# Kernel optimization log

Measured on AMD Instinct MI355X. Metric: run time of the kernel, lower is better.

Reference implementation:

```python
import jax, jax.numpy as jnp
import numpy as np

T, B, D_IN, H = 512, 256, 512, 128

def setup_inputs() -> dict:
    key = jax.random.key(0)
    ks = jax.random.split(key, 6)
    c0 = jax.random.normal(ks[0], (B, H), jnp.float32)
    h0 = jax.random.normal(ks[1], (B, H), jnp.float32)
    obs = jax.random.normal(ks[2], (T, B, D_IN), jnp.float32)
    done = jax.random.randint(ks[3], (T, B), 0, 2).astype(jnp.bool_)
    Wi = jax.random.normal(ks[4], (D_IN, 4 * H), jnp.float32) * (1.0 / np.sqrt(D_IN))
    Wh = jax.random.normal(ks[5], (H, 4 * H), jnp.float32) * (1.0 / np.sqrt(H))
    b = jnp.zeros((4 * H,), jnp.float32)
    return {"c0": c0, "h0": h0, "obs": obs, "done": done, "Wi": Wi, "Wh": Wh, "b": b}

def reference(c0, h0, obs, done, Wi, Wh, b):
    # Time-scanned flax LSTMCell with done-masked state reset.
    # Carry reset: where(done, initialize_carry()=zeros, old_state).
    # Flax LSTMCell gates (order i,f,g,o): sigmoid/sigmoid/tanh/sigmoid,
    # dense_i has no bias, dense_h has bias b.
    def step(carry, inp):
        c, h = carry
        x, d = inp                      # x: [B, D_IN], d: [B]
        keep = jnp.logical_not(d)[:, None]
        c = jnp.where(keep, c, 0.0)
        h = jnp.where(keep, h, 0.0)
        gates = x @ Wi + h @ Wh + b     # [B, 4H]
        i, f, g, o = jnp.split(gates, 4, axis=-1)
        new_c = jax.nn.sigmoid(f) * c + jax.nn.sigmoid(i) * jnp.tanh(g)
        new_h = jax.nn.sigmoid(o) * jnp.tanh(new_c)
        return (new_c, new_h), new_h

    (cT, hT), ys = jax.lax.scan(step, (c0, h0), (obs, done))
    return ys, cT, hT
```

## Files before the change

### kernel.cpp

```cpp
#include <hip/hip_runtime.h>
#include <hip/hip_bf16.h>
#include <cstdint>
#include <cstddef>

#define TT  512
#define BB  256
#define DIN 512
#define HH  128
#define NG  512

typedef __bf16 bf16x8 __attribute__((ext_vector_type(8)));
typedef float  f32x4  __attribute__((ext_vector_type(4)));

__device__ __forceinline__ float p_recip1p(float e) {
  float s = __builtin_fmaf(2.f, e, -1.f);
  float p = __builtin_fmaf(s, -0.00336424f, 0.00980413f);
  p = __builtin_fmaf(s, p, -0.0243654f);
  p = __builtin_fmaf(s, p, 0.0734565f);
  p = __builtin_fmaf(s, p, -0.222261f);
  p = __builtin_fmaf(s, p, 0.666706f);
  return p;
}
__device__ __forceinline__ float fast_sig(float x) {
  float e = __builtin_amdgcn_exp2f(-1.44269504f * __builtin_fabsf(x));
  float p = p_recip1p(e);
  return x >= 0.f ? p : 1.f - p;
}
__device__ __forceinline__ float fast_tanh(float x) {
  float e = __builtin_amdgcn_exp2f(-2.88539008f * __builtin_fabsf(x));
  float t = __builtin_fmaf(2.f, p_recip1p(e), -1.f);
  return __builtin_copysignf(t, x);
}

__device__ __forceinline__ void lgkm_barrier() {
  asm volatile("s_waitcnt lgkmcnt(0)\n\ts_barrier" ::: "memory");
}

__global__ void wconv_kernel(const float* __restrict__ Wi, const float* __restrict__ Wh,
                             __bf16* __restrict__ WiT, __bf16* __restrict__ WhT) {
  int idx = blockIdx.x * 256 + threadIdx.x;
  if (idx < DIN * NG) {
    int n = idx >> 9, k = idx & 511;
    WiT[(size_t)n * DIN + k] = (__bf16)Wi[(size_t)k * NG + n];
  }
  if (idx < HH * NG) {
    int n = idx >> 7, k = idx & 127;
    WhT[(size_t)n * HH + k] = (__bf16)Wh[(size_t)k * NG + n];
  }
}

__global__ __launch_bounds__(512, 2)
void gemm_kernel(const float* __restrict__ obs, const __bf16* __restrict__ WiT,
                 const float* __restrict__ bias, __bf16* __restrict__ Xg) {
  __shared__ __bf16 Alds[128][40];
  const int tid  = threadIdx.x;
  const int wave = tid >> 6, lane = tid & 63;
  const int l15  = lane & 15, q = lane >> 4;
  const size_t m0 = (size_t)blockIdx.x * 128;

  const f32x4 fzero = {0.f, 0.f, 0.f, 0.f};
  f32x4 acc[8][4];
#pragma unroll
  for (int i = 0; i < 8; i++)
#pragma unroll
    for (int jj = 0; jj < 4; jj++) acc[i][jj] = fzero;

  const int am = tid >> 2, aq = tid & 3;
  const float* aptr = obs + (m0 + am) * DIN + aq * 8;
  const __bf16* bptr[4];
#pragma unroll
  for (int nt = 0; nt < 4; nt++)
    bptr[nt] = WiT + (size_t)(wave * 64 + nt * 16 + l15) * DIN + q * 8;

  float4 a0[2], a1[2];
  bf16x8 bs[2][4];
  a0[0] = *(const float4*)(aptr);      a1[0] = *(const float4*)(aptr + 4);
  a0[1] = *(const float4*)(aptr + 32); a1[1] = *(const float4*)(aptr + 36);
#pragma unroll
  for (int nt = 0; nt < 4; nt++) {
    bs[0][nt] = *(const bf16x8*)(bptr[nt]);
    bs[1][nt] = *(const bf16x8*)(bptr[nt] + 32);
  }

#pragma unroll
  for (int kc = 0; kc < DIN; kc += 32) {
    const int sl = (kc >> 5) & 1;
    if (kc) lgkm_barrier();
    {
      float4 f0 = a0[sl], f1 = a1[sl];
      bf16x8 v = {(__bf16)f0.x, (__bf16)f0.y, (__bf16)f0.z, (__bf16)f0.w,
                  (__bf16)f1.x, (__bf16)f1.y, (__bf16)f1.z, (__bf16)f1.w};
      *(bf16x8*)&Alds[am][aq * 8] = v;
    }
    lgkm_barrier();
    int kp = kc + 64; if (kp > DIN - 32) kp = DIN - 32;
    a0[sl] = *(const float4*)(aptr + kp);
    a1[sl] = *(const float4*)(aptr + kp + 4);
#pragma unroll
    for (int mt = 0; mt < 8; mt++) {
      bf16x8 af = *(const bf16x8*)&Alds[mt * 16 + l15][q * 8];
#pragma unroll
      for (int nt = 0; nt < 4; nt++)
        acc[mt][nt] = __builtin_amdgcn_mfma_f32_16x16x32_bf16(af, bs[sl][nt], acc[mt][nt], 0, 0, 0);
    }
#pragma unroll
    for (int nt = 0; nt < 4; nt++)
      bs[sl][nt] = *(const bf16x8*)(bptr[nt] + kp);
  }

  const int t = blockIdx.x >> 1;
  const int half = blockIdx.x & 1;
#pragma unroll
  for (int mt = 0; mt < 8; mt++) {
    const int bg = half * 8 + mt;
#pragma unroll
    for (int nt = 0; nt < 4; nt++) {
      const int n = wave * 64 + nt * 16 + l15;
      const int g = n >> 7, jj = n & 127;
      const float bb = bias[n];
      __bf16* base = Xg + (size_t)(t * 16 + bg) * 4 * 2048 + jj * 16 + q * 4 + g;
#pragma unroll
      for (int r = 0; r < 4; r++)
        base[(size_t)r * 2048] = (__bf16)(acc[mt][nt][r] + bb);
    }
  }
}

template<int R0>
__device__ __forceinline__ void scan_body(
    const __bf16* __restrict__ Xg, const __bf16* __restrict__ WhT,
    const int* __restrict__ done, const float* __restrict__ c0,
    const float* __restrict__ h0, float* __restrict__ out,
    int bg, __bf16 (*hlds)[16][HH + 8]) {
  const int tid  = threadIdx.x;
  const int wave = tid >> 6, lane = tid & 63;
  const int l15  = lane & 15, q = lane >> 4;
  const int b0 = bg * 16;
  const int j  = wave * 16 + l15;
  const int b  = b0 + q * 4 + R0;
  const int row = q * 4 + R0;

  bf16x8 bfrag[4][4];
#pragma unroll
  for (int g = 0; g < 4; g++)
#pragma unroll
    for (int ks = 0; ks < 4; ks++)
      bfrag[g][ks] = *(const bf16x8*)(WhT + (size_t)(g * HH + j) * HH + ks * 32 + q * 8);

  for (int i = tid; i < 2 * 16 * (HH + 8); i += 512) ((__bf16*)hlds)[i] = (__bf16)0.f;
  __syncthreads();
  const int d0 = done[b];
  float c = c0[(size_t)b * HH + j];
  hlds[0][row][j] = d0 ? (__bf16)0.f : (__bf16)h0[(size_t)b * HH + j];
  __syncthreads();

  const size_t tstride = (size_t)16 * 4 * 2048;
  const __bf16* xpA = Xg + (size_t)(bg * 4 + R0) * 2048 + j * 16 + q * 4;
  const __bf16* xpB = xpA + tstride;
  const int* dpA = done + b;
  const int* dpB = dpA + BB;
  uint2 xgA = *(const uint2*)xpA;  xpA += 2 * tstride;
  uint2 xgB = *(const uint2*)xpB;  xpB += 2 * tstride;
  int dnA = *dpA; dpA += 2 * BB;
  int dnB = *dpB; dpB += 2 * BB;

  const f32x4 fz = {0.f, 0.f, 0.f, 0.f};
  float* op = out + (size_t)b * HH + j;
  float nh = 0.f;

  for (int t = 0; t < TT; t += 2) {
    {
      uint2 xg_c = xgA; int dn_c = dnA, dn_w = dnB;
      if (t + 2 < TT) { xgA = *(const uint2*)xpA; dnA = *dpA; }
      xpA += 2 * tstride; dpA += 2 * BB;

      bf16x8 af[4];
#pragma unroll
      for (int ks = 0; ks < 4; ks++)
        af[ks] = *(const bf16x8*)&hlds[0][l15][ks * 32 + q * 8];
      union { uint2 u; __bf16 h[4]; } ux; ux.u = xg_c;
      f32x4 acc[4];
#pragma unroll
      for (int g = 0; g < 4; g++) {
        float xv = (float)ux.h[g];
        acc[g] = (f32x4){xv, xv, xv, xv};
#pragma unroll
        for (int ks = 0; ks < 4; ks++)
          acc[g] = __builtin_amdgcn_mfma_f32_16x16x32_bf16(af[ks], bfrag[g][ks], acc[g], 0, 0, 0);
      }
      float gi = acc[0][R0], gf = acc[1][R0], gg = acc[2][R0], go = acc[3][R0];
      float cprev = dn_c ? 0.f : c;
      float nc = __builtin_fmaf(fast_sig(gf), cprev, fast_sig(gi) * fast_tanh(gg));
      nh = fast_sig(go) * fast_tanh(nc);
      c = nc;
      *op = nh; op += BB * HH;
      hlds[1][row][j] = dn_w ? (__bf16)0.f : (__bf16)nh;
      lgkm_barrier();
    }
    {
      uint2 xg_c = xgB; int dn_c = dnB, dn_w = dnA;
      if (t + 3 < TT) { xgB = *(const uint2*)xpB; dnB = *dpB; }
      xpB += 2 * tstride; dpB += 2 * BB;

      bf16x8 af[4];
#pragma unroll
      for (int ks = 0; ks < 4; ks++)
        af[ks] = *(const bf16x8*)&hlds[1][l15][ks * 32 + q * 8];
      union { uint2 u; __bf16 h[4]; } ux; ux.u = xg_c;
      f32x4 acc[4];
#pragma unroll
      for (int g = 0; g < 4; g++) {
        float xv = (float)ux.h[g];
        acc[g] = (f32x4){xv, xv, xv, xv};
#pragma unroll
        for (int ks = 0; ks < 4; ks++)
          acc[g] = __builtin_amdgcn_mfma_f32_16x16x32_bf16(af[ks], bfrag[g][ks], acc[g], 0, 0, 0);
      }
      float gi = acc[0][R0], gf = acc[1][R0], gg = acc[2][R0], go = acc[3][R0];
      float cprev = dn_c ? 0.f : c;
      float nc = __builtin_fmaf(fast_sig(gf), cprev, fast_sig(gi) * fast_tanh(gg));
      nh = fast_sig(go) * fast_tanh(nc);
      c = nc;
      *op = nh; op += BB * HH;
      hlds[0][row][j] = dn_w ? (__bf16)0.f : (__bf16)nh;
      lgkm_barrier();
    }
  }
  (void)fz;

  float* cT = out + (size_t)TT * BB * HH;
  float* hT = cT + (size_t)BB * HH;
  cT[(size_t)b * HH + j] = c;
  hT[(size_t)b * HH + j] = nh;
}

__global__ __launch_bounds__(512, 2)
void scan_kernel(const __bf16* __restrict__ Xg, const __bf16* __restrict__ WhT,
                 const int* __restrict__ done, const float* __restrict__ c0,
                 const float* __restrict__ h0, float* __restrict__ out) {
  __shared__ __bf16 hlds[2][16][HH + 8];
  const int bg = blockIdx.x >> 2;
  switch (blockIdx.x & 3) {
    case 0: scan_body<0>(Xg, WhT, done, c0, h0, out, bg, hlds); break;
    case 1: scan_body<1>(Xg, WhT, done, c0, h0, out, bg, hlds); break;
    case 2: scan_body<2>(Xg, WhT, done, c0, h0, out, bg, hlds); break;
    case 3: scan_body<3>(Xg, WhT, done, c0, h0, out, bg, hlds); break;
  }
}

extern "C" void kernel_launch(void* const* d_in, const int* in_sizes, int n_in,
                              void* d_out, int out_size, void* d_ws, size_t ws_size,
                              hipStream_t stream) {
  const float* c0   = (const float*)d_in[0];
  const float* h0   = (const float*)d_in[1];
  const float* obs  = (const float*)d_in[2];
  const int*   done = (const int*)d_in[3];
  const float* Wi   = (const float*)d_in[4];
  const float* Wh   = (const float*)d_in[5];
  const float* bias = (const float*)d_in[6];
  float* out = (float*)d_out;

  char* ws = (char*)d_ws;
  __bf16* Xg  = (__bf16*)ws;
  __bf16* WiT = (__bf16*)(ws + (size_t)134217728);
  __bf16* WhT = (__bf16*)(ws + (size_t)134217728 + 524288);

  wconv_kernel<<<dim3(1024), dim3(256), 0, stream>>>(Wi, Wh, WiT, WhT);
  gemm_kernel<<<dim3(1024), dim3(512), 0, stream>>>(obs, WiT, bias, Xg);
  scan_kernel<<<dim3(64), dim3(512), 0, stream>>>(Xg, WhT, done, c0, h0, out);
}
```

Before: 799.5 us.

## Fuse input GEMM and recurrent scan into one kernel with per-timestep flags

Merges the input-projection GEMM and the recurrent scan into one launch. The first 64 blocks run the scan and spin on per-timestep atomic counters that the GEMM blocks increment after writing their slice of Xg. This lets the serial scan start while the GEMM is still producing later timesteps, hiding most of the GEMM behind the scan. It also swaps the polynomial sigmoid/tanh for exp plus hardware reciprocal and splits the MFMA accumulation into two independent chains to shorten the dependency. The cost is a reliance on scan blocks being resident alongside GEMM blocks (deadlock risk if they are not) and extra atomic-load overhead on each step.

Result: faster. 774.1 us (-3.2%).

```diff
diff --git a/kernel.cpp b/kernel.cpp
--- a/kernel.cpp
+++ b/kernel.cpp
@@ -12,33 +12,37 @@
 typedef __bf16 bf16x8 __attribute__((ext_vector_type(8)));
 typedef float  f32x4  __attribute__((ext_vector_type(4)));
 
-__device__ __forceinline__ float p_recip1p(float e) {
-  float s = __builtin_fmaf(2.f, e, -1.f);
-  float p = __builtin_fmaf(s, -0.00336424f, 0.00980413f);
-  p = __builtin_fmaf(s, p, -0.0243654f);
-  p = __builtin_fmaf(s, p, 0.0734565f);
-  p = __builtin_fmaf(s, p, -0.222261f);
-  p = __builtin_fmaf(s, p, 0.666706f);
-  return p;
-}
 __device__ __forceinline__ float fast_sig(float x) {
-  float e = __builtin_amdgcn_exp2f(-1.44269504f * __builtin_fabsf(x));
-  float p = p_recip1p(e);
-  return x >= 0.f ? p : 1.f - p;
+  float e = __builtin_amdgcn_exp2f(-1.44269504f * x);
+  return __builtin_amdgcn_rcpf(1.f + e);
 }
 __device__ __forceinline__ float fast_tanh(float x) {
-  float e = __builtin_amdgcn_exp2f(-2.88539008f * __builtin_fabsf(x));
-  float t = __builtin_fmaf(2.f, p_recip1p(e), -1.f);
-  return __builtin_copysignf(t, x);
+  float e = __builtin_amdgcn_exp2f(-2.88539008f * x);
+  return __builtin_fmaf(2.f, __builtin_amdgcn_rcpf(1.f + e), -1.f);
 }
 
 __device__ __forceinline__ void lgkm_barrier() {
   asm volatile("s_waitcnt lgkmcnt(0)\n\ts_barrier" ::: "memory");
 }
 
+__device__ __forceinline__ int ld_flag(const int* p) {
+  return __hip_atomic_load(p, __ATOMIC_RELAXED, __HIP_MEMORY_SCOPE_AGENT);
+}
+__device__ __forceinline__ uint2 ld_xg8(const __bf16* p) {
+  unsigned long long v = __hip_atomic_load((const unsigned long long*)p,
+                                           __ATOMIC_RELAXED, __HIP_MEMORY_SCOPE_AGENT);
+  union { unsigned long long u; uint2 v2; } cv; cv.u = v;
+  return cv.v2;
+}
+
 __global__ void wconv_kernel(const float* __restrict__ Wi, const float* __restrict__ Wh,
-                             __bf16* __restrict__ WiT, __bf16* __restrict__ WhT) {
+                             __bf16* __restrict__ WiT, __bf16* __restrict__ WhT,
+                             int* __restrict__ flags) {
   int idx = blockIdx.x * 256 + threadIdx.x;
+  if (blockIdx.x == 0) {
+    flags[threadIdx.x] = 0;
+    flags[threadIdx.x + 256] = 0;
+  }
   if (idx < DIN * NG) {
     int n = idx >> 9, k = idx & 511;
     WiT[(size_t)n * DIN + k] = (__bf16)Wi[(size_t)k * NG + n];
@@ -49,14 +53,14 @@
   }
 }
 
-__global__ __launch_bounds__(512, 2)
-void gemm_kernel(const float* __restrict__ obs, const __bf16* __restrict__ WiT,
-                 const float* __restrict__ bias, __bf16* __restrict__ Xg) {
-  __shared__ __bf16 Alds[128][40];
+__device__ __forceinline__ void gemm_body(
+    const float* __restrict__ obs, const __bf16* __restrict__ WiT,
+    const float* __restrict__ bias, __bf16* __restrict__ Xg,
+    int* __restrict__ flags, int bid, __bf16 (*Alds)[40]) {
   const int tid  = threadIdx.x;
   const int wave = tid >> 6, lane = tid & 63;
   const int l15  = lane & 15, q = lane >> 4;
-  const size_t m0 = (size_t)blockIdx.x * 128;
+  const size_t m0 = (size_t)bid * 128;
 
   const f32x4 fzero = {0.f, 0.f, 0.f, 0.f};
   f32x4 acc[8][4];
@@ -108,8 +112,8 @@
       bs[sl][nt] = *(const bf16x8*)(bptr[nt] + kp);
   }
 
-  const int t = blockIdx.x >> 1;
-  const int half = blockIdx.x & 1;
+  const int t = bid >> 1;
+  const int half = bid & 1;
 #pragma unroll
   for (int mt = 0; mt < 8; mt++) {
     const int bg = half * 8 + mt;
@@ -124,6 +128,12 @@
         base[(size_t)r * 2048] = (__bf16)(acc[mt][nt][r] + bb);
     }
   }
+
+  __syncthreads();
+  if (tid == 0) {
+    __threadfence();
+    __hip_atomic_fetch_add(flags + t, 1, __ATOMIC_RELEASE, __HIP_MEMORY_SCOPE_AGENT);
+  }
 }
 
 template<int R0>
@@ -131,6 +141,7 @@
     const __bf16* __restrict__ Xg, const __bf16* __restrict__ WhT,
     const int* __restrict__ done, const float* __restrict__ c0,
     const float* __restrict__ h0, float* __restrict__ out,
+    const int* __restrict__ flags,
     int bg, __bf16 (*hlds)[16][HH + 8]) {
   const int tid  = threadIdx.x;
   const int wave = tid >> 6, lane = tid & 63;
@@ -159,74 +170,70 @@
   const __bf16* xpB = xpA + tstride;
   const int* dpA = done + b;
   const int* dpB = dpA + BB;
-  uint2 xgA = *(const uint2*)xpA;  xpA += 2 * tstride;
-  uint2 xgB = *(const uint2*)xpB;  xpB += 2 * tstride;
+
+  { int f = ld_flag(flags + 0); while (f < 2) f = ld_flag(flags + 0); }
+  { int f = ld_flag(flags + 1); while (f < 2) f = ld_flag(flags + 1); }
+  uint2 xgA = ld_xg8(xpA);  xpA += 2 * tstride;
+  uint2 xgB = ld_xg8(xpB);  xpB += 2 * tstride;
   int dnA = *dpA; dpA += 2 * BB;
   int dnB = *dpB; dpB += 2 * BB;
-
-  const f32x4 fz = {0.f, 0.f, 0.f, 0.f};
+  int fA = ld_flag(flags + 2);
+  int fB = ld_flag(flags + 3);
+
   float* op = out + (size_t)b * HH + j;
   float nh = 0.f;
+
+#define SCAN_STEP(XGC, DNC, DNW, RD, WR)                                      \
+  {                                                                           \
+    bf16x8 af[4];                                                             \
+    _Pragma("unroll")                                                         \
+    for (int ks = 0; ks < 4; ks++)                                            \
+      af[ks] = *(const bf16x8*)&hlds[RD][l15][ks * 32 + q * 8];               \
+    union { uint2 u; __bf16 h[4]; } ux; ux.u = (XGC);                         \
+    float gv[4];                                                              \
+    _Pragma("unroll")                                                         \
+    for (int g = 0; g < 4; g++) {                                             \
+      float xv = (float)ux.h[g];                                              \
+      f32x4 accA = {xv, xv, xv, xv};                                          \
+      accA = __builtin_amdgcn_mfma_f32_16x16x32_bf16(af[0], bfrag[g][0], accA, 0, 0, 0); \
+      accA = __builtin_amdgcn_mfma_f32_16x16x32_bf16(af[2], bfrag[g][2], accA, 0, 0, 0); \
+      f32x4 accB = {0.f, 0.f, 0.f, 0.f};                                      \
+      accB = __builtin_amdgcn_mfma_f32_16x16x32_bf16(af[1], bfrag[g][1], accB, 0, 0, 0); \
+      accB = __builtin_amdgcn_mfma_f32_16x16x32_bf16(af[3], bfrag[g][3], accB, 0, 0, 0); \
+      gv[g] = accA[R0] + accB[R0];                                            \
+    }                                                                         \
+    float cprev = (DNC) ? 0.f : c;                                            \
+    float nc = __builtin_fmaf(fast_sig(gv[1]), cprev, fast_sig(gv[0]) * fast_tanh(gv[2])); \
+    nh = fast_sig(gv[3]) * fast_tanh(nc);                                     \
+    c = nc;                                                                   \
+    hlds[WR][row][j] = (DNW) ? (__bf16)0.f : (__bf16)nh;                      \
+    *op = nh; op += BB * HH;                                                  \
+    lgkm_barrier();                                                           \
+  }
 
   for (int t = 0; t < TT; t += 2) {
     {
       uint2 xg_c = xgA; int dn_c = dnA, dn_w = dnB;
-      if (t + 2 < TT) { xgA = *(const uint2*)xpA; dnA = *dpA; }
+      if (t + 2 < TT) {
+        while (fA < 2) fA = ld_flag(flags + t + 2);
+        xgA = ld_xg8(xpA); dnA = *dpA;
+        fA = (t + 4 < TT) ? ld_flag(flags + t + 4) : 2;
+      }
       xpA += 2 * tstride; dpA += 2 * BB;
-
-      bf16x8 af[4];
-#pragma unroll
-      for (int ks = 0; ks < 4; ks++)
-        af[ks] = *(const bf16x8*)&hlds[0][l15][ks * 32 + q * 8];
-      union { uint2 u; __bf16 h[4]; } ux; ux.u = xg_c;
-      f32x4 acc[4];
-#pragma unroll
-      for (int g = 0; g < 4; g++) {
-        float xv = (float)ux.h[g];
-        acc[g] = (f32x4){xv, xv, xv, xv};
-#pragma unroll
-        for (int ks = 0; ks < 4; ks++)
-          acc[g] = __builtin_amdgcn_mfma_f32_16x16x32_bf16(af[ks], bfrag[g][ks], acc[g], 0, 0, 0);
-      }
-      float gi = acc[0][R0], gf = acc[1][R0], gg = acc[2][R0], go = acc[3][R0];
-      float cprev = dn_c ? 0.f : c;
-      float nc = __builtin_fmaf(fast_sig(gf), cprev, fast_sig(gi) * fast_tanh(gg));
-      nh = fast_sig(go) * fast_tanh(nc);
-      c = nc;
-      *op = nh; op += BB * HH;
-      hlds[1][row][j] = dn_w ? (__bf16)0.f : (__bf16)nh;
-      lgkm_barrier();
+      SCAN_STEP(xg_c, dn_c, dn_w, 0, 1)
     }
     {
       uint2 xg_c = xgB; int dn_c = dnB, dn_w = dnA;
-      if (t + 3 < TT) { xgB = *(const uint2*)xpB; dnB = *dpB; }
+      if (t + 3 < TT) {
+        while (fB < 2) fB = ld_flag(flags + t + 3);
+        xgB = ld_xg8(xpB); dnB = *dpB;
+        fB = (t + 5 < TT) ? ld_flag(flags + t + 5) : 2;
+      }
       xpB += 2 * tstride; dpB += 2 * BB;
-
-      bf16x8 af[4];
-#pragma unroll
-      for (int ks = 0; ks < 4; ks++)
-        af[ks] = *(const bf16x8*)&hlds[1][l15][ks * 32 + q * 8];
-      union { uint2 u; __bf16 h[4]; } ux; ux.u = xg_c;
-      f32x4 acc[4];
-#pragma unroll
-      for (int g = 0; g < 4; g++) {
-        float xv = (float)ux.h[g];
-        acc[g] = (f32x4){xv, xv, xv, xv};
-#pragma unroll
-        for (int ks = 0; ks < 4; ks++)
-          acc[g] = __builtin_amdgcn_mfma_f32_16x16x32_bf16(af[ks], bfrag[g][ks], acc[g], 0, 0, 0);
-      }
-      float gi = acc[0][R0], gf = acc[1][R0], gg = acc[2][R0], go = acc[3][R0];
-      float cprev = dn_c ? 0.f : c;
-      float nc = __builtin_fmaf(fast_sig(gf), cprev, fast_sig(gi) * fast_tanh(gg));
-      nh = fast_sig(go) * fast_tanh(nc);
-      c = nc;
-      *op = nh; op += BB * HH;
-      hlds[0][row][j] = dn_w ? (__bf16)0.f : (__bf16)nh;
-      lgkm_barrier();
-    }
-  }
-  (void)fz;
+      SCAN_STEP(xg_c, dn_c, dn_w, 1, 0)
+    }
+  }
+#undef SCAN_STEP
 
   float* cT = out + (size_t)TT * BB * HH;
   float* hT = cT + (size_t)BB * HH;
@@ -235,16 +242,23 @@
 }
 
 __global__ __launch_bounds__(512, 2)
-void scan_kernel(const __bf16* __restrict__ Xg, const __bf16* __restrict__ WhT,
-                 const int* __restrict__ done, const float* __restrict__ c0,
-                 const float* __restrict__ h0, float* __restrict__ out) {
-  __shared__ __bf16 hlds[2][16][HH + 8];
-  const int bg = blockIdx.x >> 2;
-  switch (blockIdx.x & 3) {
-    case 0: scan_body<0>(Xg, WhT, done, c0, h0, out, bg, hlds); break;
-    case 1: scan_body<1>(Xg, WhT, done, c0, h0, out, bg, hlds); break;
-    case 2: scan_body<2>(Xg, WhT, done, c0, h0, out, bg, hlds); break;
-    case 3: scan_body<3>(Xg, WhT, done, c0, h0, out, bg, hlds); break;
+void fused_kernel(const float* __restrict__ obs, const __bf16* __restrict__ WiT,
+                  const float* __restrict__ bias, __bf16* __restrict__ Xg,
+                  const __bf16* __restrict__ WhT, const int* __restrict__ done,
+                  const float* __restrict__ c0, const float* __restrict__ h0,
+                  float* __restrict__ out, int* __restrict__ flags) {
+  __shared__ __align__(16) char smem[10240];
+  if (blockIdx.x < 64) {
+    __bf16 (*hlds)[16][HH + 8] = (__bf16 (*)[16][HH + 8])smem;
+    const int bg = blockIdx.x >> 2;
+    switch (blockIdx.x & 3) {
+      case 0: scan_body<0>(Xg, WhT, done, c0, h0, out, flags, bg, hlds); break;
+      case 1: scan_body<1>(Xg, WhT, done, c0, h0, out, flags, bg, hlds); break;
+      case 2: scan_body<2>(Xg, WhT, done, c0, h0, out, flags, bg, hlds); break;
+      case 3: scan_body<3>(Xg, WhT, done, c0, h0, out, flags, bg, hlds); break;
+    }
+  } else {
+    gemm_body(obs, WiT, bias, Xg, flags, blockIdx.x - 64, (__bf16 (*)[40])smem);
   }
 }
 
@@ -264,8 +278,9 @@
   __bf16* Xg  = (__bf16*)ws;
   __bf16* WiT = (__bf16*)(ws + (size_t)134217728);
   __bf16* WhT = (__bf16*)(ws + (size_t)134217728 + 524288);
-
-  wconv_kernel<<<dim3(1024), dim3(256), 0, stream>>>(Wi, Wh, WiT, WhT);
-  gemm_kernel<<<dim3(1024), dim3(512), 0, stream>>>(obs, WiT, bias, Xg);
-  scan_kernel<<<dim3(64), dim3(512), 0, stream>>>(Xg, WhT, done, c0, h0, out);
-}
+  int*  flags = (int*)(ws + (size_t)134217728 + 524288 + 131072);
+
+  wconv_kernel<<<dim3(1024), dim3(256), 0, stream>>>(Wi, Wh, WiT, WhT, flags);
+  fused_kernel<<<dim3(1088), dim3(512), 0, stream>>>(obs, WiT, bias, Xg, WhT, done,
+                                                     c0, h0, out, flags);
+}
```
